# Optimization experiments

Measured on AMD Instinct MI355X. Metric: run time of the kernel, lower is better.

Reference implementation:

```python
import jax, jax.numpy as jnp
import numpy as np

SIGMA = 0.1
GAMMA = 1.0 / (SIGMA * SIGMA)  # keops-style gauss kernel: exp(-|x-y|^2 / sigma^2)
B, N, D = 1, 8192, 3


def setup_inputs() -> dict:
    key = jax.random.key(0)
    k1, k2 = jax.random.split(key)
    control_points = jax.random.uniform(k1, (B, N, D), dtype=jnp.float32)
    mom = jax.random.normal(k2, (B, N, D), dtype=jnp.float32) * 0.1
    return {"mom": mom, "control_points": control_points}


def _pairwise_dist2(x, y):
    # x:[B,N,D], y:[B,M,D] -> [B,N,M] squared distances (no N x M x D intermediate)
    x2 = jnp.sum(x * x, -1)  # [B,N]
    y2 = jnp.sum(y * y, -1)  # [B,M]
    xy = jnp.einsum('bnd,bmd->bnm', x, y)
    return x2[:, :, None] + y2[:, None, :] - 2.0 * xy


def gauss_kernel(x, y, b):
    # K(x,y) b : [B,N,d]
    K = jnp.exp(-GAMMA * _pairwise_dist2(x, y))  # [B,N,M]
    return jnp.einsum('bnm,bmd->bnd', K, b)


def gauss_grad_kernel(p, x):
    # dH/dx_i = sum_j d/dx_i[exp(-g|x_i-x_j|^2)] <p_i,p_j>
    #         = -2g * sum_j K_ij <p_i,p_j> (x_i - x_j)
    K = jnp.exp(-GAMMA * _pairwise_dist2(x, x))        # [B,N,N]
    W = K * jnp.einsum('bnd,bmd->bnm', p, p)           # [B,N,N] weighted by <p_i,p_j>
    row_sum = jnp.sum(W, -1)                           # [B,N]
    Wx = jnp.einsum('bnm,bmd->bnd', W, x)              # [B,N,D]
    return (-2.0 * GAMMA) * (x * row_sum[:, :, None] - Wx)


def reference(mom, control_points):
    # variational_evolve: (dp/dt, dx/dt)
    dmom = -gauss_grad_kernel(mom, control_points)
    dx = gauss_kernel(control_points, control_points, mom)
    return (dmom, dx)
```

## Files before the change

### kernel.cpp

```cpp
#include <hip/hip_runtime.h>


#define TPB 256
#define GAMMA_F 100.0f

__global__ __launch_bounds__(TPB) void lddmm_evolve_kernel(
    const float* __restrict__ mom,
    const float* __restrict__ xpt,
    float* __restrict__ out,
    int N) {
  const int i    = blockIdx.x * TPB + threadIdx.x;
  const int jb   = blockIdx.y * TPB;

  __shared__ float sx[TPB], sy[TPB], sz[TPB];
  __shared__ float spx[TPB], spy[TPB], spz[TPB];

  {
    const int j = jb + threadIdx.x;
    sx[threadIdx.x]  = xpt[3 * j + 0];
    sy[threadIdx.x]  = xpt[3 * j + 1];
    sz[threadIdx.x]  = xpt[3 * j + 2];
    spx[threadIdx.x] = mom[3 * j + 0];
    spy[threadIdx.x] = mom[3 * j + 1];
    spz[threadIdx.x] = mom[3 * j + 2];
  }
  __syncthreads();

  const float xi = xpt[3 * i + 0], yi = xpt[3 * i + 1], zi = xpt[3 * i + 2];
  const float pxi = mom[3 * i + 0], pyi = mom[3 * i + 1], pzi = mom[3 * i + 2];

  float a = 0.f;
  float wx = 0.f, wy = 0.f, wz = 0.f;
  float gx = 0.f, gy = 0.f, gz = 0.f;

#pragma unroll 8
  for (int j = 0; j < TPB; ++j) {
    const float bx = sx[j], by = sy[j], bz = sz[j];
    const float qx = spx[j], qy = spy[j], qz = spz[j];
    const float dx = xi - bx, dy = yi - by, dz = zi - bz;
    const float d2 = dx * dx + dy * dy + dz * dz;
    const float K = __expf(-GAMMA_F * d2);
    const float dot = pxi * qx + pyi * qy + pzi * qz;
    const float w = K * dot;
    a  += w;
    wx += w * bx; wy += w * by; wz += w * bz;
    gx += K * qx; gy += K * qy; gz += K * qz;
  }

  const float c = 2.0f * GAMMA_F;
  atomicAdd(&out[3 * i + 0], c * (xi * a - wx));
  atomicAdd(&out[3 * i + 1], c * (yi * a - wy));
  atomicAdd(&out[3 * i + 2], c * (zi * a - wz));
  atomicAdd(&out[3 * N + 3 * i + 0], gx);
  atomicAdd(&out[3 * N + 3 * i + 1], gy);
  atomicAdd(&out[3 * N + 3 * i + 2], gz);
}

extern "C" void kernel_launch(void* const* d_in, const int* in_sizes, int n_in,
                              void* d_out, int out_size, void* d_ws, size_t ws_size,
                              hipStream_t stream) {
  const float* mom = (const float*)d_in[0];
  const float* xpt = (const float*)d_in[1];
  float* out = (float*)d_out;
  const int N = in_sizes[0] / 3;

  hipMemsetAsync(d_out, 0, (size_t)out_size * sizeof(float), stream);

  dim3 grid(N / TPB, N / TPB);
  lddmm_evolve_kernel<<<grid, TPB, 0, stream>>>(mom, xpt, out, N);
}
```

Measured before the change: 102.6 us.

## Replace atomics with segmented partial sums and exp2-folded distance expansion

Splits the j-range into SEG segments whose per-row partial sums are written to workspace and combined by separate reduce and finalize kernels. This replaces the memset plus atomicAdd accumulation. The inner loop now precomputes scaled positions and squared norms into float4 shared memory, so the exponent argument is a chain of FMAs fed to exp2f, with the log2e scaling undone in finalize. The costs are two extra kernel launches and workspace traffic, and the expanded distance form may lose some precision for nearby points.

```diff
diff --git a/kernel.cpp b/kernel.cpp
--- a/kernel.cpp
+++ b/kernel.cpp
@@ -2,58 +2,127 @@
 
 
 #define TPB 256
-#define GAMMA_F 100.0f
+constexpr float GAMMA_C = 100.0f;
+constexpr float LOG2E_C = 1.4426950408889634f;
+constexpr float SB_C    = 2.0f * GAMMA_C * LOG2E_C;
+constexpr float SC_C    = -GAMMA_C * LOG2E_C;
+constexpr float LN2_C   = 0.69314718055994531f;
 
-__global__ __launch_bounds__(TPB) void lddmm_evolve_kernel(
-    const float* __restrict__ mom,
-    const float* __restrict__ xpt,
-    float* __restrict__ out,
-    int N) {
-  const int i    = blockIdx.x * TPB + threadIdx.x;
-  const int jb   = blockIdx.y * TPB;
+__global__ __launch_bounds__(TPB, 8) void lddmm_partial(
+    const float* __restrict__ mom, const float* __restrict__ xpt,
+    float* __restrict__ ws, int N, int SEG, int JT) {
+  extern __shared__ float4 smem[];
+  float4* sA = smem;
+  float4* sP = smem + JT;
+  const int tid = threadIdx.x;
+  const int seg = blockIdx.y;
 
-  __shared__ float sx[TPB], sy[TPB], sz[TPB];
-  __shared__ float spx[TPB], spy[TPB], spz[TPB];
-
-  {
-    const int j = jb + threadIdx.x;
-    sx[threadIdx.x]  = xpt[3 * j + 0];
-    sy[threadIdx.x]  = xpt[3 * j + 1];
-    sz[threadIdx.x]  = xpt[3 * j + 2];
-    spx[threadIdx.x] = mom[3 * j + 0];
-    spy[threadIdx.x] = mom[3 * j + 1];
-    spz[threadIdx.x] = mom[3 * j + 2];
+  for (int t = tid; t < JT; t += TPB) {
+    const int j = seg * JT + t;
+    const float bx = xpt[3*j], by = xpt[3*j+1], bz = xpt[3*j+2];
+    sA[t] = make_float4(SB_C*bx, SB_C*by, SB_C*bz,
+                        SC_C * fmaf(bx, bx, fmaf(by, by, bz*bz)));
+    sP[t] = make_float4(mom[3*j], mom[3*j+1], mom[3*j+2], 0.f);
   }
   __syncthreads();
 
-  const float xi = xpt[3 * i + 0], yi = xpt[3 * i + 1], zi = xpt[3 * i + 2];
-  const float pxi = mom[3 * i + 0], pyi = mom[3 * i + 1], pzi = mom[3 * i + 2];
+  const int i = blockIdx.x * TPB + tid;
+  const float xi  = xpt[3*i], yi  = xpt[3*i+1], zi  = xpt[3*i+2];
+  const float pxi = mom[3*i], pyi = mom[3*i+1], pzi = mom[3*i+2];
+  const float ci  = SC_C * fmaf(xi, xi, fmaf(yi, yi, zi*zi));
 
   float a = 0.f;
   float wx = 0.f, wy = 0.f, wz = 0.f;
   float gx = 0.f, gy = 0.f, gz = 0.f;
 
-#pragma unroll 8
-  for (int j = 0; j < TPB; ++j) {
-    const float bx = sx[j], by = sy[j], bz = sz[j];
-    const float qx = spx[j], qy = spy[j], qz = spz[j];
-    const float dx = xi - bx, dy = yi - by, dz = zi - bz;
-    const float d2 = dx * dx + dy * dy + dz * dz;
-    const float K = __expf(-GAMMA_F * d2);
-    const float dot = pxi * qx + pyi * qy + pzi * qz;
-    const float w = K * dot;
+#pragma unroll 4
+  for (int t = 0; t < JT; ++t) {
+    const float4 A = sA[t];
+    const float4 P = sP[t];
+    const float arg = fmaf(A.x, xi, fmaf(A.y, yi, fmaf(A.z, zi, ci + A.w)));
+    const float K   = exp2f(arg);
+    const float dot = fmaf(P.x, pxi, fmaf(P.y, pyi, P.z * pzi));
+    const float w   = K * dot;
     a  += w;
-    wx += w * bx; wy += w * by; wz += w * bz;
-    gx += K * qx; gy += K * qy; gz += K * qz;
+    wx = fmaf(w, A.x, wx); wy = fmaf(w, A.y, wy); wz = fmaf(w, A.z, wz);
+    gx = fmaf(K, P.x, gx); gy = fmaf(K, P.y, gy); gz = fmaf(K, P.z, gz);
   }
 
-  const float c = 2.0f * GAMMA_F;
-  atomicAdd(&out[3 * i + 0], c * (xi * a - wx));
-  atomicAdd(&out[3 * i + 1], c * (yi * a - wy));
-  atomicAdd(&out[3 * i + 2], c * (zi * a - wz));
-  atomicAdd(&out[3 * N + 3 * i + 0], gx);
-  atomicAdd(&out[3 * N + 3 * i + 1], gy);
-  atomicAdd(&out[3 * N + 3 * i + 2], gz);
+  const size_t SN = (size_t)SEG * N;
+  float* p = ws + (size_t)seg * N + i;
+  p[0*SN] = a;
+  p[1*SN] = wx; p[2*SN] = wy; p[3*SN] = wz;
+  p[4*SN] = gx; p[5*SN] = gy; p[6*SN] = gz;
+}
+
+__global__ __launch_bounds__(TPB) void lddmm_reduce(
+    const float* __restrict__ ws, float* __restrict__ R, int N, int SEG) {
+  const int i = blockIdx.x * TPB + threadIdx.x;
+  const int c = blockIdx.y;
+  const float* src = ws + (size_t)c * SEG * N + i;
+  float s0 = 0.f, s1 = 0.f, s2 = 0.f, s3 = 0.f;
+  int s = 0;
+  for (; s + 4 <= SEG; s += 4) {
+    s0 += src[(size_t)(s+0)*N]; s1 += src[(size_t)(s+1)*N];
+    s2 += src[(size_t)(s+2)*N]; s3 += src[(size_t)(s+3)*N];
+  }
+  for (; s < SEG; ++s) s0 += src[(size_t)s*N];
+  R[(size_t)c * N + i] = (s0 + s1) + (s2 + s3);
+}
+
+__global__ __launch_bounds__(TPB) void lddmm_finalize(
+    const float* __restrict__ R, const float* __restrict__ xpt,
+    float* __restrict__ out, int N) {
+  const int i = blockIdx.x * TPB + threadIdx.x;
+  const float A  = R[i];
+  const float WX = R[(size_t)1*N+i], WY = R[(size_t)2*N+i], WZ = R[(size_t)3*N+i];
+  const float GX = R[(size_t)4*N+i], GY = R[(size_t)5*N+i], GZ = R[(size_t)6*N+i];
+  const float xi = xpt[3*i], yi = xpt[3*i+1], zi = xpt[3*i+2];
+  const float TGA = 2.0f * GAMMA_C * A;
+  out[3*i+0] = fmaf(TGA, xi, -LN2_C * WX);
+  out[3*i+1] = fmaf(TGA, yi, -LN2_C * WY);
+  out[3*i+2] = fmaf(TGA, zi, -LN2_C * WZ);
+  out[3*N + 3*i + 0] = GX;
+  out[3*N + 3*i + 1] = GY;
+  out[3*N + 3*i + 2] = GZ;
+}
+
+__global__ __launch_bounds__(TPB) void lddmm_atomic(
+    const float* __restrict__ mom, const float* __restrict__ xpt,
+    float* __restrict__ out, int N) {
+  const int i  = blockIdx.x * TPB + threadIdx.x;
+  const int jb = blockIdx.y * TPB;
+  __shared__ float4 sA[TPB], sP[TPB];
+  {
+    const int j = jb + threadIdx.x;
+    const float bx = xpt[3*j], by = xpt[3*j+1], bz = xpt[3*j+2];
+    sA[threadIdx.x] = make_float4(SB_C*bx, SB_C*by, SB_C*bz,
+                                  SC_C * fmaf(bx, bx, fmaf(by, by, bz*bz)));
+    sP[threadIdx.x] = make_float4(mom[3*j], mom[3*j+1], mom[3*j+2], 0.f);
+  }
+  __syncthreads();
+  const float xi = xpt[3*i], yi = xpt[3*i+1], zi = xpt[3*i+2];
+  const float pxi = mom[3*i], pyi = mom[3*i+1], pzi = mom[3*i+2];
+  const float ci = SC_C * fmaf(xi, xi, fmaf(yi, yi, zi*zi));
+  float a=0.f, wx=0.f, wy=0.f, wz=0.f, gx=0.f, gy=0.f, gz=0.f;
+#pragma unroll 4
+  for (int t = 0; t < TPB; ++t) {
+    const float4 A = sA[t], P = sP[t];
+    const float arg = fmaf(A.x, xi, fmaf(A.y, yi, fmaf(A.z, zi, ci + A.w)));
+    const float K   = exp2f(arg);
+    const float dot = fmaf(P.x, pxi, fmaf(P.y, pyi, P.z * pzi));
+    const float w   = K * dot;
+    a += w;
+    wx = fmaf(w, A.x, wx); wy = fmaf(w, A.y, wy); wz = fmaf(w, A.z, wz);
+    gx = fmaf(K, P.x, gx); gy = fmaf(K, P.y, gy); gz = fmaf(K, P.z, gz);
+  }
+  const float TGA = 2.0f * GAMMA_C * a;
+  atomicAdd(&out[3*i+0], fmaf(TGA, xi, -LN2_C * wx));
+  atomicAdd(&out[3*i+1], fmaf(TGA, yi, -LN2_C * wy));
+  atomicAdd(&out[3*i+2], fmaf(TGA, zi, -LN2_C * wz));
+  atomicAdd(&out[3*N+3*i+0], gx);
+  atomicAdd(&out[3*N+3*i+1], gy);
+  atomicAdd(&out[3*N+3*i+2], gz);
 }
 
 extern "C" void kernel_launch(void* const* d_in, const int* in_sizes, int n_in,
@@ -64,8 +133,23 @@
   float* out = (float*)d_out;
   const int N = in_sizes[0] / 3;
 
-  hipMemsetAsync(d_out, 0, (size_t)out_size * sizeof(float), stream);
+  auto need = [&](int s) { return (size_t)(7*s + 7) * (size_t)N * sizeof(float); };
+  int SEG = 64;
+  while (SEG > 2 && need(SEG) > ws_size) SEG >>= 1;
 
-  dim3 grid(N / TPB, N / TPB);
-  lddmm_evolve_kernel<<<grid, TPB, 0, stream>>>(mom, xpt, out, N);
+  if (need(SEG) <= ws_size) {
+    const int JT = N / SEG;
+    float* wsf = (float*)d_ws;
+    float* R   = wsf + (size_t)7 * SEG * N;
+    const size_t shmem = (size_t)JT * 2 * sizeof(float4);
+    dim3 gA(N / TPB, SEG);
+    lddmm_partial<<<gA, TPB, shmem, stream>>>(mom, xpt, wsf, N, SEG, JT);
+    dim3 gB(N / TPB, 7);
+    lddmm_reduce<<<gB, TPB, 0, stream>>>(wsf, R, N, SEG);
+    lddmm_finalize<<<N / TPB, TPB, 0, stream>>>(R, xpt, out, N);
+  } else {
+    hipMemsetAsync(d_out, 0, (size_t)out_size * sizeof(float), stream);
+    dim3 grid(N / TPB, N / TPB);
+    lddmm_atomic<<<grid, TPB, 0, stream>>>(mom, xpt, out, N);
+  }
 }
```

After: 107.1 us. 1.04x slower.
